# Optimization experiments

Hardware: AMD Instinct MI355X
Metric: run time of the kernel (lower is better)

The kernel has to match this reference:

```python
import jax, jax.numpy as jnp
import numpy as np

N, D_IN, D_OUT = 4096, 1024, 1024

def setup_inputs() -> dict:
    key = jax.random.key(0)
    ks = jax.random.split(key, 7)
    s = 1.0 / np.sqrt(D_IN)
    return {
        "x": jax.random.normal(ks[0], (N, D_IN), dtype=jnp.float32),
        "W1": jax.random.normal(ks[1], (D_OUT, D_IN), dtype=jnp.float32) * s,
        "b1": jax.random.normal(ks[2], (D_OUT,), dtype=jnp.float32) * 0.01,
        "W2": jax.random.normal(ks[3], (D_OUT, D_IN), dtype=jnp.float32) * s,
        "b2": jax.random.normal(ks[4], (D_OUT,), dtype=jnp.float32) * 0.01,
        "W3": jax.random.normal(ks[5], (D_OUT, D_IN), dtype=jnp.float32) * s,
        "b3": jax.random.normal(ks[6], (D_OUT,), dtype=jnp.float32) * 0.01,
        "output_dim": D_OUT,
    }

def reference(x, W1, b1, W2, b2, W3, b3, output_dim):
    # q, k, v: [N, D_OUT]  (torch Linear: x @ W.T + b)
    q = x @ W1.T + b1
    k = x @ W2.T + b2
    v = x @ W3.T + b3
    # NOTE: original computes K @ Q^T (not Q @ K^T) — keep faithful.
    scale = 1.0 / jnp.sqrt(jnp.asarray(output_dim, dtype=x.dtype))
    attn = jax.nn.softmax(jnp.einsum("nd,md->nm", k, q) * scale, axis=-1)  # [N, N]
    # value.unsqueeze(0) * attn.unsqueeze(-1) summed over axis 1 == attn @ v
    return attn @ v  # [N, D_OUT]
```

## Files before the change

### kernel.cpp

```cpp
#include <hip/hip_runtime.h>


typedef short bf16x8 __attribute__((ext_vector_type(8)));
typedef float f32x4  __attribute__((ext_vector_type(4)));

__device__ __forceinline__ short f2bf(float f) {
    unsigned u = __builtin_bit_cast(unsigned, f);
    u += 0x7FFFu + ((u >> 16) & 1u);
    return (short)(u >> 16);
}
__device__ __forceinline__ float bf2f(short s) {
    return __builtin_bit_cast(float, (unsigned)((unsigned short)s) << 16);
}

__device__ __forceinline__ void gld_lds16(const short* g, short* l) {
    __builtin_amdgcn_global_load_lds(
        (const __attribute__((address_space(1))) void*)g,
        (__attribute__((address_space(3))) void*)l, 16, 0, 0);
}

template<int BM, int BN>
__global__ __launch_bounds__(256)
void gemm_bt(const short* __restrict__ A, int lda,
             const short* __restrict__ B, int ldb,
             const float* __restrict__ bias, int bias_mode,
             void* __restrict__ Cout, int ldc, int c_fp32, float scale,
             int K)
{
    constexpr int NT = BN / 32;
    __shared__ __align__(16) short As[BM * 64];
    __shared__ __align__(16) short Bs[BN * 64];

    const int tid  = threadIdx.x;
    const int lane = tid & 63;
    const int wave = tid >> 6;
    const int wm   = (wave >> 1) * 64;
    const int wn   = (wave & 1) * (BN / 2);
    const int quad = lane >> 4;
    const int l16  = lane & 15;
    const size_t bm0 = (size_t)blockIdx.y * BM;
    const size_t bn0 = (size_t)blockIdx.x * BN;

    f32x4 acc[4][NT] = {};

    const int srow = lane >> 3;
    const int scol = ((lane & 7) ^ srow) << 3;
    const short* Ag = A + (bm0 + srow) * (size_t)lda + scol;
    const short* Bg = B + (bn0 + srow) * (size_t)ldb + scol;

    for (int k0 = 0; k0 < K; k0 += 64) {
#pragma unroll
        for (int cc = 0; cc < BM / 8; cc += 4) {
            const int c = cc + wave;
            gld_lds16(Ag + (size_t)c * 8 * lda + k0, &As[c * 512]);
        }
#pragma unroll
        for (int cc = 0; cc < BN / 8; cc += 4) {
            const int c = cc + wave;
            gld_lds16(Bg + (size_t)c * 8 * ldb + k0, &Bs[c * 512]);
        }
        __syncthreads();

        bf16x8 af[2][4], bfr[2][NT];
#pragma unroll
        for (int ks = 0; ks < 2; ks++) {
            const int sw = (ks << 2) + quad;
#pragma unroll
            for (int mt = 0; mt < 4; mt++) {
                const int r = wm + mt * 16 + l16;
                af[ks][mt] = *(const bf16x8*)(&As[r * 64 + ((sw ^ (r & 7)) << 3)]);
            }
#pragma unroll
            for (int nt = 0; nt < NT; nt++) {
                const int r = wn + nt * 16 + l16;
                bfr[ks][nt] = *(const bf16x8*)(&Bs[r * 64 + ((sw ^ (r & 7)) << 3)]);
            }
        }
#pragma unroll
        for (int ks = 0; ks < 2; ks++)
#pragma unroll
            for (int mt = 0; mt < 4; mt++)
#pragma unroll
                for (int nt = 0; nt < NT; nt++)
                    acc[mt][nt] = __builtin_amdgcn_mfma_f32_16x16x32_bf16(
                        af[ks][mt], bfr[ks][nt], acc[mt][nt], 0, 0, 0);
        __syncthreads();
    }

#pragma unroll
    for (int mt = 0; mt < 4; mt++) {
#pragma unroll
        for (int nt = 0; nt < NT; nt++) {
            const size_t col = bn0 + wn + nt * 16 + l16;
            const float bcol = (bias_mode == 1) ? bias[col] : 0.0f;
#pragma unroll
            for (int r = 0; r < 4; r++) {
                const size_t row = bm0 + wm + mt * 16 + quad * 4 + r;
                float v = acc[mt][nt][r] * scale + bcol;
                if (bias_mode == 2) v += bias[row];
                if (c_fp32) ((float*)Cout)[row * (size_t)ldc + col] = v;
                else        ((short*)Cout)[row * (size_t)ldc + col] = f2bf(v);
            }
        }
    }
}

__global__ __launch_bounds__(256)
void softmax_rows_bf16(short* __restrict__ P)
{
    short* p = P + (size_t)blockIdx.x * 4096;
    const int tid = threadIdx.x;
    const int wave = tid >> 6, lane = tid & 63;
    const int base = tid << 4;

    short sh[16];
    *(int4*)(sh)     = *(const int4*)(p + base);
    *(int4*)(sh + 8) = *(const int4*)(p + base + 8);

    float v[16];
    float mx = -1e30f;
#pragma unroll
    for (int i = 0; i < 16; i++) { v[i] = bf2f(sh[i]); mx = fmaxf(mx, v[i]); }
#pragma unroll
    for (int off = 32; off; off >>= 1) mx = fmaxf(mx, __shfl_down(mx, off));
    __shared__ float red[4];
    if (lane == 0) red[wave] = mx;
    __syncthreads();
    mx = fmaxf(fmaxf(red[0], red[1]), fmaxf(red[2], red[3]));

    float sum = 0.0f;
#pragma unroll
    for (int i = 0; i < 16; i++) { v[i] = __expf(v[i] - mx); sum += v[i]; }
#pragma unroll
    for (int off = 32; off; off >>= 1) sum += __shfl_down(sum, off);
    __syncthreads();
    if (lane == 0) red[wave] = sum;
    __syncthreads();
    const float inv = 1.0f / (red[0] + red[1] + red[2] + red[3]);

#pragma unroll
    for (int i = 0; i < 16; i++) sh[i] = f2bf(v[i] * inv);
    *(int4*)(p + base)     = *(const int4*)(sh);
    *(int4*)(p + base + 8) = *(const int4*)(sh + 8);
}

__global__ __launch_bounds__(256)
void cast4(const float* __restrict__ in, short* __restrict__ out, int n4)
{
    const int i = blockIdx.x * 256 + threadIdx.x;
    if (i >= n4) return;
    const float4 f = ((const float4*)in)[i];
    short4 o;
    o.x = f2bf(f.x); o.y = f2bf(f.y); o.z = f2bf(f.z); o.w = f2bf(f.w);
    ((short4*)out)[i] = o;
}

__global__ __launch_bounds__(256)
void cast_w3(const float* __restrict__ W1, const float* __restrict__ W2,
             const float* __restrict__ W3, short* __restrict__ out, int per4)
{
    const int i = blockIdx.x * 256 + threadIdx.x;
    if (i >= 3 * per4) return;
    const float* src = (i < per4) ? W1 : (i < 2 * per4 ? W2 : W3);
    const int j = (i < per4) ? i : (i < 2 * per4 ? i - per4 : i - 2 * per4);
    const float4 f = ((const float4*)src)[j];
    short4 o;
    o.x = f2bf(f.x); o.y = f2bf(f.y); o.z = f2bf(f.z); o.w = f2bf(f.w);
    ((short4*)out)[i] = o;
}

__global__ __launch_bounds__(256)
void bias_cat2(const float* __restrict__ b1, const float* __restrict__ b2,
               float* __restrict__ cat, int n)
{
    const int i = blockIdx.x * 256 + threadIdx.x;
    if (i < n) cat[i] = b1[i];
    else if (i < 2 * n) cat[i] = b2[i - n];
}

extern "C" void kernel_launch(void* const* d_in, const int* in_sizes, int n_in,
                              void* d_out, int out_size, void* d_ws, size_t ws_size,
                              hipStream_t stream)
{
    const float* x  = (const float*)d_in[0];
    const float* W1 = (const float*)d_in[1];
    const float* b1 = (const float*)d_in[2];
    const float* W2 = (const float*)d_in[3];
    const float* b2 = (const float*)d_in[4];
    const float* W3 = (const float*)d_in[5];
    const float* b3 = (const float*)d_in[6];
    float* out = (float*)d_out;

    const int N = 4096, D = 1024;

    short* xb   = (short*)d_ws;
    short* Wb   = xb + (size_t)N * D;
    float* bcat = (float*)(Wb + (size_t)3 * D * D);
    short* qk   = (short*)(bcat + 2 * D);
    short* vt   = qk + (size_t)N * 2 * D;
    short* S    = vt + (size_t)N * D;

    cast4<<<(N * D / 4) / 256, 256, 0, stream>>>(x, xb, N * D / 4);
    cast_w3<<<(3 * D * D / 4) / 256, 256, 0, stream>>>(W1, W2, W3, Wb, D * D / 4);
    bias_cat2<<<(2 * D + 255) / 256, 256, 0, stream>>>(b1, b2, bcat, D);

    dim3 gqk(2 * D / 128, N / 128);
    gemm_bt<128, 128><<<gqk, 256, 0, stream>>>(xb, D, Wb, D, bcat, 1,
                                               qk, 2 * D, 0, 1.0f, D);

    dim3 gvt(N / 64, D / 128);
    gemm_bt<128, 64><<<gvt, 256, 0, stream>>>(Wb + (size_t)2 * D * D, D, xb, D,
                                              b3, 2, vt, N, 0, 1.0f, D);

    dim3 gs(N / 128, N / 128);
    gemm_bt<128, 128><<<gs, 256, 0, stream>>>(qk + D, 2 * D, qk, 2 * D,
                                              nullptr, 0, S, N, 0, 0.03125f, D);

    softmax_rows_bf16<<<N, 256, 0, stream>>>(S);

    dim3 go(D / 64, N / 128);
    gemm_bt<128, 64><<<go, 256, 0, stream>>>(S, N, vt, N,
                                             nullptr, 0, out, D, 1, 1.0f, N);
}
```

Measured before the change: 264.6 us.

## Fuse QKV projection, transpose V separately, split-K final GEMM with reduction

```diff
diff --git a/kernel.cpp b/kernel.cpp
--- a/kernel.cpp
+++ b/kernel.cpp
@@ -25,7 +25,7 @@
              const short* __restrict__ B, int ldb,
              const float* __restrict__ bias, int bias_mode,
              void* __restrict__ Cout, int ldc, int c_fp32, float scale,
-             int K)
+             int K, size_t zstride)
 {
     constexpr int NT = BN / 32;
     __shared__ __align__(16) short As[BM * 64];
@@ -40,13 +40,14 @@
     const int l16  = lane & 15;
     const size_t bm0 = (size_t)blockIdx.y * BM;
     const size_t bn0 = (size_t)blockIdx.x * BN;
+    const int koff = blockIdx.z * K;
 
     f32x4 acc[4][NT] = {};
 
     const int srow = lane >> 3;
     const int scol = ((lane & 7) ^ srow) << 3;
-    const short* Ag = A + (bm0 + srow) * (size_t)lda + scol;
-    const short* Bg = B + (bn0 + srow) * (size_t)ldb + scol;
+    const short* Ag = A + (bm0 + srow) * (size_t)lda + koff + scol;
+    const short* Bg = B + (bn0 + srow) * (size_t)ldb + koff + scol;
 
     for (int k0 = 0; k0 < K; k0 += 64) {
 #pragma unroll
@@ -87,6 +88,8 @@
         __syncthreads();
     }
 
+    float* Cf = (float*)Cout + blockIdx.z * zstride;
+    short* Cs = (short*)Cout + blockIdx.z * zstride;
 #pragma unroll
     for (int mt = 0; mt < 4; mt++) {
 #pragma unroll
@@ -98,8 +101,8 @@
                 const size_t row = bm0 + wm + mt * 16 + quad * 4 + r;
                 float v = acc[mt][nt][r] * scale + bcol;
                 if (bias_mode == 2) v += bias[row];
-                if (c_fp32) ((float*)Cout)[row * (size_t)ldc + col] = v;
-                else        ((short*)Cout)[row * (size_t)ldc + col] = f2bf(v);
+                if (c_fp32) Cf[row * (size_t)ldc + col] = v;
+                else        Cs[row * (size_t)ldc + col] = f2bf(v);
             }
         }
     }
@@ -142,6 +145,39 @@
     for (int i = 0; i < 16; i++) sh[i] = f2bf(v[i] * inv);
     *(int4*)(p + base)     = *(const int4*)(sh);
     *(int4*)(p + base + 8) = *(const int4*)(sh + 8);
+}
+
+__global__ __launch_bounds__(256)
+void transpose_v(const short* __restrict__ qkv, short* __restrict__ vt)
+{
+    __shared__ short sh[64][72];
+    const int n0 = blockIdx.x * 64, d0 = blockIdx.y * 64;
+    const int t = threadIdx.x;
+    const int r = t >> 2, c = (t & 3) << 4;
+
+    const short* src = qkv + (size_t)(n0 + r) * 3072 + 2048 + d0 + c;
+    *(int4*)(&sh[r][c])     = *(const int4*)(src);
+    *(int4*)(&sh[r][c + 8]) = *(const int4*)(src + 8);
+    __syncthreads();
+
+    short tmp[16];
+#pragma unroll
+    for (int j = 0; j < 16; j++) tmp[j] = sh[c + j][r];
+    short* dst = vt + (size_t)(d0 + r) * 4096 + n0 + c;
+    *(int4*)(dst)     = *(const int4*)(tmp);
+    *(int4*)(dst + 8) = *(const int4*)(tmp + 8);
+}
+
+__global__ __launch_bounds__(256)
+void reduce2(const float* __restrict__ p, float* __restrict__ out, int n4)
+{
+    const int i = blockIdx.x * 256 + threadIdx.x;
+    if (i >= n4) return;
+    const float4 a = ((const float4*)p)[i];
+    const float4 b = ((const float4*)(p + (size_t)4096 * 1024))[i];
+    float4 o;
+    o.x = a.x + b.x; o.y = a.y + b.y; o.z = a.z + b.z; o.w = a.w + b.w;
+    ((float4*)out)[i] = o;
 }
 
 __global__ __launch_bounds__(256)
@@ -170,12 +206,13 @@
 }
 
 __global__ __launch_bounds__(256)
-void bias_cat2(const float* __restrict__ b1, const float* __restrict__ b2,
-               float* __restrict__ cat, int n)
+void bias_cat3(const float* __restrict__ b1, const float* __restrict__ b2,
+               const float* __restrict__ b3, float* __restrict__ cat, int n)
 {
     const int i = blockIdx.x * 256 + threadIdx.x;
     if (i < n) cat[i] = b1[i];
     else if (i < 2 * n) cat[i] = b2[i - n];
+    else if (i < 3 * n) cat[i] = b3[i - 2 * n];
 }
 
 extern "C" void kernel_launch(void* const* d_in, const int* in_sizes, int n_in,
@@ -196,29 +233,33 @@
     short* xb   = (short*)d_ws;
     short* Wb   = xb + (size_t)N * D;
     float* bcat = (float*)(Wb + (size_t)3 * D * D);
-    short* qk   = (short*)(bcat + 2 * D);
-    short* vt   = qk + (size_t)N * 2 * D;
+    short* qkv  = (short*)(bcat + 3 * D);
+    short* vt   = qkv + (size_t)N * 3 * D;
     short* S    = vt + (size_t)N * D;
+    float* outp = (float*)d_ws;
 
     cast4<<<(N * D / 4) / 256, 256, 0, stream>>>(x, xb, N * D / 4);
     cast_w3<<<(3 * D * D / 4) / 256, 256, 0, stream>>>(W1, W2, W3, Wb, D * D / 4);
-    bias_cat2<<<(2 * D + 255) / 256, 256, 0, stream>>>(b1, b2, bcat, D);
-
-    dim3 gqk(2 * D / 128, N / 128);
-    gemm_bt<128, 128><<<gqk, 256, 0, stream>>>(xb, D, Wb, D, bcat, 1,
-                                               qk, 2 * D, 0, 1.0f, D);
-
-    dim3 gvt(N / 64, D / 128);
-    gemm_bt<128, 64><<<gvt, 256, 0, stream>>>(Wb + (size_t)2 * D * D, D, xb, D,
-                                              b3, 2, vt, N, 0, 1.0f, D);
+    bias_cat3<<<(3 * D + 255) / 256, 256, 0, stream>>>(b1, b2, b3, bcat, D);
+
+    dim3 gqkv(3 * D / 128, N / 128);
+    gemm_bt<128, 128><<<gqkv, 256, 0, stream>>>(xb, D, Wb, D, bcat, 1,
+                                                qkv, 3 * D, 0, 1.0f, D, 0);
+
+    dim3 gt(N / 64, D / 64);
+    transpose_v<<<gt, 256, 0, stream>>>(qkv, vt);
 
     dim3 gs(N / 128, N / 128);
-    gemm_bt<128, 128><<<gs, 256, 0, stream>>>(qk + D, 2 * D, qk, 2 * D,
-                                              nullptr, 0, S, N, 0, 0.03125f, D);
+    gemm_bt<128, 128><<<gs, 256, 0, stream>>>(qkv + D, 3 * D, qkv, 3 * D,
+                                              nullptr, 0, S, N, 0, 0.03125f,
+                                              D, 0);
 
     softmax_rows_bf16<<<N, 256, 0, stream>>>(S);
 
-    dim3 go(D / 64, N / 128);
-    gemm_bt<128, 64><<<go, 256, 0, stream>>>(S, N, vt, N,
-                                             nullptr, 0, out, D, 1, 1.0f, N);
-}
+    dim3 go(D / 64, N / 128, 2);
+    gemm_bt<128, 64><<<go, 256, 0, stream>>>(S, N, vt, N, nullptr, 0,
+                                             outp, D, 1, 1.0f, N / 2,
+                                             (size_t)N * D);
+
+    reduce2<<<(N * D / 4) / 256, 256, 0, stream>>>(outp, out, N * D / 4);
+}
```

Measured after the change: 259.5 us. About the same (-1.9%).
